# Kernel optimization log

Hardware: AMD Instinct MI355X
Metric: run time of the kernel (lower is better)

The kernel has to match this reference:

```python
import jax, jax.numpy as jnp
import numpy as np

B, T = 2, 1024
V, D, H, L = 32000, 1024, 16, 8
DH = D // H  # 64
ROPE_BASE = 1000.0
EPS = 1e-6


def _rms_norm(x):
    # F.rms_norm(x, (C,), eps=1e-6)
    ms = jnp.mean(jnp.square(x), axis=-1, keepdims=True)
    return x * jax.lax.rsqrt(ms + EPS)


def _rope_tables(t_len):
    quarter = DH // 4
    inv_freq = jnp.concatenate([
        ROPE_BASE ** (-jnp.arange(quarter, dtype=jnp.float32) / quarter),
        jnp.zeros(quarter, dtype=jnp.float32),
    ])  # [DH/2]
    theta = jnp.arange(t_len, dtype=jnp.float32)[:, None] * inv_freq[None, :]  # [T, DH/2]
    return jnp.cos(theta), jnp.sin(theta)


def _apply_rope(x, cos, sin):
    # x: [B, H, T, DH]; cos/sin: [T, DH/2] broadcast to [1,1,T,DH/2]
    half = DH // 2
    x1, x2 = x[..., :half], x[..., half:]
    c = cos[None, None]
    s = sin[None, None]
    return jnp.concatenate([c * x1 - s * x2, s * x1 + c * x2], axis=-1).astype(x.dtype)


def setup_inputs() -> dict:
    key = jax.random.key(0)
    ks = jax.random.split(key, 7)
    s = 0.02
    return {
        "x_indices": jax.random.randint(ks[0], (B, T), 0, V, dtype=jnp.int32),
        "embedding": jax.random.normal(ks[1], (V, D), dtype=jnp.float32) * s,
        "Wqkv": jax.random.normal(ks[2], (L, 3 * D, D), dtype=jnp.float32) * s,
        "Wout": jax.random.normal(ks[3], (L, D, D), dtype=jnp.float32) * s,
        "W1": jax.random.normal(ks[4], (L, 4 * D, D), dtype=jnp.float32) * s,
        "W2": jax.random.normal(ks[5], (L, D, 4 * D), dtype=jnp.float32) * s,
        "lm_head": jax.random.normal(ks[6], (V, D), dtype=jnp.float32) * s,
    }


def reference(x_indices, embedding, Wqkv, Wout, W1, W2, lm_head):
    x = embedding[x_indices]  # [B, T, D]
    cos, sin = _rope_tables(T)
    causal = jnp.tril(jnp.ones((T, T), dtype=bool))  # [T, T]
    neg = jnp.finfo(x.dtype).min
    scale = 1.0 / np.sqrt(DH)

    for l in range(L):
        n = _rms_norm(x)
        qkv = jnp.einsum('btd,ed->bte', n, Wqkv[l])  # [B, T, 3D]
        qkv = qkv.reshape(B, T, 3, H, DH)
        q = jnp.transpose(qkv[:, :, 0], (0, 2, 1, 3))  # [B, H, T, DH]
        k = jnp.transpose(qkv[:, :, 1], (0, 2, 1, 3))
        v = jnp.transpose(qkv[:, :, 2], (0, 2, 1, 3))
        q = _apply_rope(q, cos, sin)
        k = _apply_rope(k, cos, sin)
        scores = jnp.einsum('bhqd,bhkd->bhqk', q, k) * scale
        scores = jnp.where(causal[None, None], scores, neg)
        attn = jax.nn.softmax(scores, axis=-1)
        ctx = jnp.einsum('bhqk,bhkd->bhqd', attn, v)
        ctx = jnp.transpose(ctx, (0, 2, 1, 3)).reshape(B, T, D)
        x = x + jnp.einsum('btd,ed->bte', ctx, Wout[l])
        n = _rms_norm(x)
        h = jnp.square(jax.nn.relu(jnp.einsum('btd,fd->btf', n, W1[l])))  # [B, T, 4D]
        x = x + jnp.einsum('btf,df->btd', h, W2[l])

    logits = jnp.einsum('btd,vd->btv', _rms_norm(x), lm_head)
    return logits.astype(jnp.float32)
```

## Files before the change

### kernel.cpp

```cpp
#include <hip/hip_runtime.h>
#include <hip/hip_bf16.h>
#include <cmath>
#include <cstdint>

#define B_  2
#define T_  1024
#define V_  32000
#define D_  1024
#define H_  16
#define L_  8
#define DH_ 64

typedef __attribute__((ext_vector_type(8))) short bf16x8;
typedef __attribute__((ext_vector_type(4))) float f32x4;

__device__ __forceinline__ ushort f2bf(float f) {
    union { float f; uint32_t u; } v; v.f = f;
    uint32_t r = v.u + 0x7FFFu + ((v.u >> 16) & 1u);
    return (ushort)(r >> 16);
}
__device__ __forceinline__ float bf2f(ushort u) {
    union { uint32_t u; float f; } v; v.u = ((uint32_t)u) << 16;
    return v.f;
}

__device__ __forceinline__ void async_copy16(const void* g, void* l) {
    __builtin_amdgcn_global_load_lds(
        (const __attribute__((address_space(1))) void*)g,
        (__attribute__((address_space(3))) void*)l, 16, 0, 0);
}

__global__ __launch_bounds__(256) void k_cast(const float4* __restrict__ in,
                                              ushort4* __restrict__ out, int n4) {
    for (int i = blockIdx.x * 256 + threadIdx.x; i < n4; i += gridDim.x * 256) {
        float4 v = in[i];
        out[i] = make_ushort4(f2bf(v.x), f2bf(v.y), f2bf(v.z), f2bf(v.w));
    }
}

__global__ void k_rope_tables(float* __restrict__ cosT, float* __restrict__ sinT) {
    int t = blockIdx.x;
    int i = threadIdx.x;
    float invf = (i < 16) ? powf(1000.0f, -(float)i / 16.0f) : 0.0f;
    float th = (float)t * invf;
    cosT[t * 32 + i] = cosf(th);
    sinT[t * 32 + i] = sinf(th);
}

__global__ __launch_bounds__(256) void k_gather(const int* __restrict__ idx,
                                                const float* __restrict__ emb,
                                                float* __restrict__ x) {
    int row = blockIdx.x;
    int id = idx[row];
    const float4* src = (const float4*)(emb + (size_t)id * D_);
    float4* dst = (float4*)(x + (size_t)row * D_);
    dst[threadIdx.x] = src[threadIdx.x];
}

__global__ __launch_bounds__(256) void k_rmsnorm(const float* __restrict__ x,
                                                 ushort* __restrict__ out) {
    int row = blockIdx.x;
    const float4* xr = (const float4*)(x + (size_t)row * D_);
    float4 v = xr[threadIdx.x];
    float ss = v.x * v.x + v.y * v.y + v.z * v.z + v.w * v.w;
    #pragma unroll
    for (int off = 1; off < 64; off <<= 1) ss += __shfl_xor(ss, off);
    __shared__ float wsum[4];
    int lane = threadIdx.x & 63, wv = threadIdx.x >> 6;
    if (lane == 0) wsum[wv] = ss;
    __syncthreads();
    float tot = wsum[0] + wsum[1] + wsum[2] + wsum[3];
    float inv = rsqrtf(tot * (1.0f / D_) + 1e-6f);
    ushort4 r = make_ushort4(f2bf(v.x * inv), f2bf(v.y * inv), f2bf(v.z * inv), f2bf(v.w * inv));
    *(ushort4*)(out + (size_t)row * D_ + threadIdx.x * 4) = r;
}

template<int BN, int EPI, bool OUTBF, bool CONVB>
__global__ __launch_bounds__(256) void k_mfma_gemm(const ushort* __restrict__ A,
                                                   const void* __restrict__ Wp,
                                                   void* __restrict__ Cp,
                                                   const float* __restrict__ Res,
                                                   const float* __restrict__ cosT,
                                                   const float* __restrict__ sinT,
                                                   int M, int N, int K) {
    constexpr int BM = 128;
    constexpr int MI = 4;
    constexpr int NI = BN / 32;
    __shared__ ushort As[BM][64];
    __shared__ ushort Bs[BN][64];
    const int tid = threadIdx.x;
    const int wid = tid >> 6, lane = tid & 63;
    const int wr = wid >> 1, wc = wid & 1;
    const int r16 = lane & 15, kc = lane >> 4;
    const int rx = (r16 & 7) << 4;
    const size_t bm = (size_t)blockIdx.x * BM;
    const size_t bn = (size_t)blockIdx.y * BN;
    const int srow = tid >> 3;
    const int sdcp = tid & 7;

    f32x4 acc[MI][NI];
    #pragma unroll
    for (int mi = 0; mi < MI; mi++)
        #pragma unroll
        for (int ni = 0; ni < NI; ni++) {
            f32x4 z = {0.f, 0.f, 0.f, 0.f};
            acc[mi][ni] = z;
        }

    for (int k0 = 0; k0 < K; k0 += 64) {
        #pragma unroll
        for (int i = 0; i < 4; i++) {
            const int row = i * 32 + srow;
            const ushort* g = A + (bm + row) * (size_t)K + k0 + ((sdcp ^ (row & 7)) * 8);
            async_copy16(g, (char*)As + (i * 256 + tid) * 16);
        }
        if constexpr (!CONVB) {
            const ushort* Wb = (const ushort*)Wp;
            #pragma unroll
            for (int i = 0; i < BN / 32; i++) {
                const int row = i * 32 + srow;
                const ushort* g = Wb + (bn + row) * (size_t)K + k0 + ((sdcp ^ (row & 7)) * 8);
                async_copy16(g, (char*)Bs + (i * 256 + tid) * 16);
            }
        } else {
            const float* Wf = (const float*)Wp;
            #pragma unroll
            for (int i = 0; i < BN / 32; i++) {
                const int row = i * 32 + srow;
                const float* src = Wf + (bn + row) * (size_t)K + k0 + sdcp * 8;
                float4 v0 = *(const float4*)(src);
                float4 v1 = *(const float4*)(src + 4);
                union { ushort u[8]; bf16x8 v; } tmp;
                tmp.u[0] = f2bf(v0.x); tmp.u[1] = f2bf(v0.y);
                tmp.u[2] = f2bf(v0.z); tmp.u[3] = f2bf(v0.w);
                tmp.u[4] = f2bf(v1.x); tmp.u[5] = f2bf(v1.y);
                tmp.u[6] = f2bf(v1.z); tmp.u[7] = f2bf(v1.w);
                *(bf16x8*)((char*)Bs + row * 128 + ((sdcp ^ (row & 7)) << 4)) = tmp.v;
            }
        }
        __syncthreads();

        #pragma unroll
        for (int kk = 0; kk < 2; kk++) {
            bf16x8 af[MI], bfr[NI];
            #pragma unroll
            for (int mi = 0; mi < MI; mi++)
                af[mi] = *(const bf16x8*)((const char*)As + (wr * 64 + mi * 16 + r16) * 128 +
                                          ((kk * 64 + kc * 16) ^ rx));
            #pragma unroll
            for (int ni = 0; ni < NI; ni++)
                bfr[ni] = *(const bf16x8*)((const char*)Bs + (wc * (BN / 2) + ni * 16 + r16) * 128 +
                                           ((kk * 64 + kc * 16) ^ rx));
            #pragma unroll
            for (int mi = 0; mi < MI; mi++)
                #pragma unroll
                for (int ni = 0; ni < NI; ni++)
                    acc[mi][ni] = __builtin_amdgcn_mfma_f32_16x16x32_bf16(af[mi], bfr[ni],
                                                                          acc[mi][ni], 0, 0, 0);
        }
        __syncthreads();
    }

    #pragma unroll
    for (int mi = 0; mi < MI; mi++) {
        #pragma unroll
        for (int j = 0; j < 4; j++) {
            const size_t row = bm + wr * 64 + mi * 16 + (lane >> 4) * 4 + j;
            if constexpr (EPI == 3) {
                static_assert(BN == 128, "rope epilogue assumes BN=128");
                const int sec = (int)((bn + wc * 64) >> 10);
                if (sec < 2) {
                    const int t = (int)(row & (T_ - 1));
                    #pragma unroll
                    for (int np = 0; np < 2; np++) {
                        const int i1 = np * 16 + r16;
                        float c = cosT[t * 32 + i1], s = sinT[t * 32 + i1];
                        float x1 = acc[mi][np][j], x2 = acc[mi][np + 2][j];
                        acc[mi][np][j]     = c * x1 - s * x2;
                        acc[mi][np + 2][j] = s * x1 + c * x2;
                    }
                }
            }
            #pragma unroll
            for (int ni = 0; ni < NI; ni++) {
                const size_t col = bn + wc * (BN / 2) + ni * 16 + r16;
                float v = acc[mi][ni][j];
                if constexpr (EPI == 1) v += Res[row * N + col];
                if constexpr (EPI == 2) { v = fmaxf(v, 0.f); v *= v; }
                if constexpr (OUTBF) ((ushort*)Cp)[row * N + col] = f2bf(v);
                else                 ((float*)Cp)[row * N + col] = v;
            }
        }
    }
}

__global__ __launch_bounds__(256) void k_attn_mfma(const ushort* __restrict__ qkv,
                                                   ushort* __restrict__ ctx) {
    __shared__ __align__(16) char lds[24576];
    const int tid = threadIdx.x;
    const int w = tid >> 6, lane = tid & 63;
    const int r16 = lane & 15, kc = lane >> 4;
    const int qb = blockIdx.x * 64;
    const int bh = blockIdx.y, b = bh >> 4, h = bh & 15;
    const size_t tok0 = (size_t)b * T_;
    const ushort* qg = qkv + (tok0 + qb) * (3 * D_) + h * DH_;
    const ushort* kg = qkv + tok0 * (3 * D_) + D_ + h * DH_;
    const ushort* vg = qkv + tok0 * (3 * D_) + 2 * D_ + h * DH_;
    const float SCALE_LOG2E = 0.125f * 1.44269504089f;

    #pragma unroll
    for (int i = 0; i < 2; i++) {
        int slot = i * 256 + tid;
        int row = slot >> 3, dcp = slot & 7;
        int d0 = (dcp ^ (row & 7)) * 8;
        async_copy16(qg + (size_t)row * (3 * D_) + d0, lds + 16384 + slot * 16);
    }
    __syncthreads();
    bf16x8 aq[2];
    #pragma unroll
    for (int ks = 0; ks < 2; ks++) {
        int row = w * 16 + r16;
        aq[ks] = *(const bf16x8*)(lds + 16384 + row * 128 + ((ks * 64 + kc * 16) ^ ((row & 7) << 4)));
    }

    f32x4 o[4];
    float m[4], l[4], corr[4];
    #pragma unroll
    for (int nd = 0; nd < 4; nd++) { f32x4 z = {0.f, 0.f, 0.f, 0.f}; o[nd] = z; }
    #pragma unroll
    for (int j = 0; j < 4; j++) { m[j] = -1e30f; l[j] = 0.f; }

    const int nch = (qb >> 6) + 1;
    for (int ch = 0; ch < nch; ch++) {
        const int kb = ch << 6;
        __syncthreads();
        #pragma unroll
        for (int i = 0; i < 2; i++) {
            int slot = i * 256 + tid;
            int row = slot >> 3, dcp = slot & 7;
            int d0 = (dcp ^ (row & 7)) * 8;
            async_copy16(kg + (size_t)(kb + row) * (3 * D_) + d0, lds + slot * 16);
        }
        {
            int key = tid >> 2, dbase = (tid & 3) * 16;
            const ushort* src = vg + (size_t)(kb + key) * (3 * D_) + dbase;
            bf16x8 v0 = *(const bf16x8*)(src);
            bf16x8 v1 = *(const bf16x8*)(src + 8);
            #pragma unroll
            for (int e = 0; e < 8; e++) {
                int d = dbase + e;
                *(ushort*)(lds + 8192 + d * 128 + ((key * 2) ^ ((d & 7) << 4))) = (ushort)v0[e];
                d = dbase + 8 + e;
                *(ushort*)(lds + 8192 + d * 128 + ((key * 2) ^ ((d & 7) << 4))) = (ushort)v1[e];
            }
        }
        __syncthreads();

        f32x4 s[4];
        #pragma unroll
        for (int ni = 0; ni < 4; ni++) { f32x4 z = {0.f, 0.f, 0.f, 0.f}; s[ni] = z; }
        __builtin_amdgcn_s_setprio(1);
        #pragma unroll
        for (int ks = 0; ks < 2; ks++)
            #pragma unroll
            for (int ni = 0; ni < 4; ni++) {
                int row = ni * 16 + r16;
                bf16x8 kf = *(const bf16x8*)(lds + row * 128 + ((ks * 64 + kc * 16) ^ ((row & 7) << 4)));
                s[ni] = __builtin_amdgcn_mfma_f32_16x16x32_bf16(aq[ks], kf, s[ni], 0, 0, 0);
            }
        __builtin_amdgcn_s_setprio(0);

        const bool diag = (kb == qb);
        #pragma unroll
        for (int j = 0; j < 4; j++) {
            const int qrow = qb + w * 16 + kc * 4 + j;
            #pragma unroll
            for (int ni = 0; ni < 4; ni++) {
                float v = s[ni][j] * SCALE_LOG2E;
                if (diag) { int key = kb + ni * 16 + r16; if (key > qrow) v = -1e30f; }
                s[ni][j] = v;
            }
            float t = fmaxf(fmaxf(s[0][j], s[1][j]), fmaxf(s[2][j], s[3][j]));
            #pragma unroll
            for (int off = 1; off < 16; off <<= 1) t = fmaxf(t, __shfl_xor(t, off));
            float mn = fmaxf(m[j], t);
            corr[j] = exp2f(m[j] - mn);
            m[j] = mn;
            float ps = 0.f;
            #pragma unroll
            for (int ni = 0; ni < 4; ni++) {
                float p = exp2f(s[ni][j] - mn);
                s[ni][j] = p;
                ps += p;
            }
            #pragma unroll
            for (int off = 1; off < 16; off <<= 1) ps += __shfl_xor(ps, off);
            l[j] = l[j] * corr[j] + ps;
        }
        #pragma unroll
        for (int ni = 0; ni < 4; ni++)
            #pragma unroll
            for (int j = 0; j < 4; j++) {
                int row = w * 16 + kc * 4 + j;
                *(ushort*)(lds + 16384 + row * 128 + ((ni * 32 + r16 * 2) ^ ((row & 7) << 4))) = f2bf(s[ni][j]);
            }
        #pragma unroll
        for (int nd = 0; nd < 4; nd++)
            #pragma unroll
            for (int j = 0; j < 4; j++) o[nd][j] *= corr[j];
        __builtin_amdgcn_s_setprio(1);
        #pragma unroll
        for (int ks = 0; ks < 2; ks++) {
            int prow = w * 16 + r16;
            bf16x8 pf = *(const bf16x8*)(lds + 16384 + prow * 128 + ((ks * 64 + kc * 16) ^ ((prow & 7) << 4)));
            #pragma unroll
            for (int nd = 0; nd < 4; nd++) {
                int drow = nd * 16 + r16;
                bf16x8 vf = *(const bf16x8*)(lds + 8192 + drow * 128 + ((ks * 64 + kc * 16) ^ ((drow & 7) << 4)));
                o[nd] = __builtin_amdgcn_mfma_f32_16x16x32_bf16(pf, vf, o[nd], 0, 0, 0);
            }
        }
        __builtin_amdgcn_s_setprio(0);
    }

    #pragma unroll
    for (int j = 0; j < 4; j++) {
        float inv = 1.0f / l[j];
        int row = qb + w * 16 + kc * 4 + j;
        ushort* dst = ctx + (tok0 + row) * D_ + h * DH_;
        #pragma unroll
        for (int nd = 0; nd < 4; nd++)
            dst[nd * 16 + r16] = f2bf(o[nd][j] * inv);
    }
}

extern "C" void kernel_launch(void* const* d_in, const int* in_sizes, int n_in,
                              void* d_out, int out_size, void* d_ws, size_t ws_size,
                              hipStream_t stream) {
    const int*   xi   = (const int*)d_in[0];
    const float* emb  = (const float*)d_in[1];
    const float* Wqkv = (const float*)d_in[2];
    const float* Wout = (const float*)d_in[3];
    const float* W1   = (const float*)d_in[4];
    const float* W2   = (const float*)d_in[5];
    const float* lmh  = (const float*)d_in[6];
    float* out = (float*)d_out;

    const size_t NT = (size_t)B_ * T_;
    size_t off = 0;
    auto carve = [&](size_t bytes) -> char* {
        char* r = (char*)d_ws + off;
        off += (bytes + 255) & ~(size_t)255;
        return r;
    };
    float*  xbuf = (float*)carve(NT * D_ * 4);
    ushort* qkv  = (ushort*)carve(NT * 3 * D_ * 2);
    ushort* nb   = (ushort*)carve(NT * D_ * 2);
    ushort* ctxb = (ushort*)carve(NT * D_ * 2);
    ushort* hb   = (ushort*)carve(NT * 4 * D_ * 2);
    float*  cosT = (float*)carve(T_ * 32 * 4);
    float*  sinT = (float*)carve(T_ * 32 * 4);

    const size_t nWqkv = (size_t)L_ * 3 * D_ * D_;
    const size_t nWout = (size_t)L_ * D_ * D_;
    const size_t nW1   = (size_t)L_ * 4 * D_ * D_;
    const size_t nW2   = (size_t)L_ * 4 * D_ * D_;
    const size_t nLmh  = (size_t)V_ * D_;
    ushort* WqkvB = (ushort*)carve(nWqkv * 2);
    ushort* WoutB = (ushort*)carve(nWout * 2);
    ushort* W1B   = (ushort*)carve(nW1 * 2);
    ushort* W2B   = (ushort*)carve(nW2 * 2);
    ushort* lmhB  = (ushort*)carve(nLmh * 2);
    const bool preconv = (off <= ws_size);

    if (preconv) {
        k_cast<<<dim3(2048), dim3(256), 0, stream>>>((const float4*)Wqkv, (ushort4*)WqkvB, (int)(nWqkv / 4));
        k_cast<<<dim3(2048), dim3(256), 0, stream>>>((const float4*)Wout, (ushort4*)WoutB, (int)(nWout / 4));
        k_cast<<<dim3(2048), dim3(256), 0, stream>>>((const float4*)W1,   (ushort4*)W1B,   (int)(nW1 / 4));
        k_cast<<<dim3(2048), dim3(256), 0, stream>>>((const float4*)W2,   (ushort4*)W2B,   (int)(nW2 / 4));
        k_cast<<<dim3(2048), dim3(256), 0, stream>>>((const float4*)lmh,  (ushort4*)lmhB,  (int)(nLmh / 4));
    }

#define LAUNCH_GEMM(BN, EPI, OUTBF, GX, GY, Aq, Wb16, Wf32, Cq, Rq, Mv, Nv, Kv)              \
    do {                                                                                     \
        if (preconv)                                                                         \
            k_mfma_gemm<BN, EPI, OUTBF, false><<<dim3(GX, GY), dim3(256), 0, stream>>>(      \
                (const ushort*)(Aq), (const void*)(Wb16), (void*)(Cq), (Rq), cosT, sinT,     \
                Mv, Nv, Kv);                                                                 \
        else                                                                                 \
            k_mfma_gemm<BN, EPI, OUTBF, true><<<dim3(GX, GY), dim3(256), 0, stream>>>(       \
                (const ushort*)(Aq), (const void*)(Wf32), (void*)(Cq), (Rq), cosT, sinT,     \
                Mv, Nv, Kv);                                                                 \
    } while (0)

    k_rope_tables<<<dim3(T_), dim3(32), 0, stream>>>(cosT, sinT);
    k_gather<<<dim3(NT), dim3(256), 0, stream>>>(xi, emb, xbuf);

    for (int l = 0; l < L_; l++) {
        k_rmsnorm<<<dim3(NT), dim3(256), 0, stream>>>(xbuf, nb);
        LAUNCH_GEMM(128, 3, true, 16, 24, nb,
                    WqkvB + (size_t)l * 3 * D_ * D_, Wqkv + (size_t)l * 3 * D_ * D_,
                    qkv, nullptr, (int)NT, 3 * D_, D_);
        k_attn_mfma<<<dim3(T_ / 64, B_ * H_), dim3(256), 0, stream>>>(qkv, ctxb);
        LAUNCH_GEMM(64, 1, false, 16, 16, ctxb,
                    WoutB + (size_t)l * D_ * D_, Wout + (size_t)l * D_ * D_,
                    xbuf, xbuf, (int)NT, D_, D_);
        k_rmsnorm<<<dim3(NT), dim3(256), 0, stream>>>(xbuf, nb);
        LAUNCH_GEMM(128, 2, true, 16, 32, nb,
                    W1B + (size_t)l * 4 * D_ * D_, W1 + (size_t)l * 4 * D_ * D_,
                    hb, nullptr, (int)NT, 4 * D_, D_);
        LAUNCH_GEMM(64, 1, false, 16, 16, hb,
                    W2B + (size_t)l * 4 * D_ * D_, W2 + (size_t)l * 4 * D_ * D_,
                    xbuf, xbuf, (int)NT, D_, 4 * D_);
    }
    k_rmsnorm<<<dim3(NT), dim3(256), 0, stream>>>(xbuf, nb);
    LAUNCH_GEMM(128, 0, false, 16, 250, nb, lmhB, lmh, out, nullptr, (int)NT, V_, D_);
#undef LAUNCH_GEMM
}
```

Measured before the change: 1.995 ms.

## Double-buffer GEMM LDS tiles, swizzle workgroup order, nontemporal fp32 output stores

The MFMA GEMM now uses two LDS buffers per operand and issues the next K-tile's loads before computing on the current one, so global-to-LDS traffic can overlap with MFMA work. Workgroup IDs are remapped in groups of eight to change which tiles run at the same time, aiming for better L2 reuse. Plain fp32 outputs (EPI 0, such as the logits) are written with nontemporal stores to avoid polluting the cache. The cost is double the LDS use, which can lower occupancy.

```diff
diff --git a/kernel.cpp b/kernel.cpp
--- a/kernel.cpp
+++ b/kernel.cpp
@@ -86,47 +86,42 @@
     constexpr int BM = 128;
     constexpr int MI = 4;
     constexpr int NI = BN / 32;
-    __shared__ ushort As[BM][64];
-    __shared__ ushort Bs[BN][64];
+    __shared__ ushort As[2][BM][64];
+    __shared__ ushort Bs[2][BN][64];
     const int tid = threadIdx.x;
     const int wid = tid >> 6, lane = tid & 63;
     const int wr = wid >> 1, wc = wid & 1;
     const int r16 = lane & 15, kc = lane >> 4;
     const int rx = (r16 & 7) << 4;
-    const size_t bm = (size_t)blockIdx.x * BM;
-    const size_t bn = (size_t)blockIdx.y * BN;
-    const int srow = tid >> 3;
+    const int srow8 = tid >> 3;
     const int sdcp = tid & 7;
 
-    f32x4 acc[MI][NI];
-    #pragma unroll
-    for (int mi = 0; mi < MI; mi++)
-        #pragma unroll
-        for (int ni = 0; ni < NI; ni++) {
-            f32x4 z = {0.f, 0.f, 0.f, 0.f};
-            acc[mi][ni] = z;
-        }
-
-    for (int k0 = 0; k0 < K; k0 += 64) {
+    const int nwg = gridDim.x * gridDim.y;
+    int orig = blockIdx.y * gridDim.x + blockIdx.x;
+    int swz = (nwg & 7) ? orig : ((orig & 7) * (nwg >> 3) + (orig >> 3));
+    const size_t bm = (size_t)(swz % gridDim.x) * BM;
+    const size_t bn = (size_t)(swz / gridDim.x) * BN;
+
+    auto stage = [&](int buf, int k0) {
         #pragma unroll
         for (int i = 0; i < 4; i++) {
-            const int row = i * 32 + srow;
+            const int row = i * 32 + srow8;
             const ushort* g = A + (bm + row) * (size_t)K + k0 + ((sdcp ^ (row & 7)) * 8);
-            async_copy16(g, (char*)As + (i * 256 + tid) * 16);
+            async_copy16(g, (char*)As + buf * (BM * 128) + (i * 256 + tid) * 16);
         }
         if constexpr (!CONVB) {
             const ushort* Wb = (const ushort*)Wp;
             #pragma unroll
             for (int i = 0; i < BN / 32; i++) {
-                const int row = i * 32 + srow;
+                const int row = i * 32 + srow8;
                 const ushort* g = Wb + (bn + row) * (size_t)K + k0 + ((sdcp ^ (row & 7)) * 8);
-                async_copy16(g, (char*)Bs + (i * 256 + tid) * 16);
+                async_copy16(g, (char*)Bs + buf * (BN * 128) + (i * 256 + tid) * 16);
             }
         } else {
             const float* Wf = (const float*)Wp;
             #pragma unroll
             for (int i = 0; i < BN / 32; i++) {
-                const int row = i * 32 + srow;
+                const int row = i * 32 + srow8;
                 const float* src = Wf + (bn + row) * (size_t)K + k0 + sdcp * 8;
                 float4 v0 = *(const float4*)(src);
                 float4 v1 = *(const float4*)(src + 4);
@@ -135,21 +130,38 @@
                 tmp.u[2] = f2bf(v0.z); tmp.u[3] = f2bf(v0.w);
                 tmp.u[4] = f2bf(v1.x); tmp.u[5] = f2bf(v1.y);
                 tmp.u[6] = f2bf(v1.z); tmp.u[7] = f2bf(v1.w);
-                *(bf16x8*)((char*)Bs + row * 128 + ((sdcp ^ (row & 7)) << 4)) = tmp.v;
-            }
-        }
-        __syncthreads();
-
+                *(bf16x8*)((char*)Bs + buf * (BN * 128) + row * 128 + ((sdcp ^ (row & 7)) << 4)) = tmp.v;
+            }
+        }
+    };
+
+    f32x4 acc[MI][NI];
+    #pragma unroll
+    for (int mi = 0; mi < MI; mi++)
+        #pragma unroll
+        for (int ni = 0; ni < NI; ni++) {
+            f32x4 z = {0.f, 0.f, 0.f, 0.f};
+            acc[mi][ni] = z;
+        }
+
+    const int KSTEPS = K >> 6;
+    stage(0, 0);
+    __syncthreads();
+    for (int step = 0; step < KSTEPS; ++step) {
+        const int cur = step & 1;
+        if (step + 1 < KSTEPS) stage(cur ^ 1, (step + 1) << 6);
         #pragma unroll
         for (int kk = 0; kk < 2; kk++) {
             bf16x8 af[MI], bfr[NI];
             #pragma unroll
             for (int mi = 0; mi < MI; mi++)
-                af[mi] = *(const bf16x8*)((const char*)As + (wr * 64 + mi * 16 + r16) * 128 +
+                af[mi] = *(const bf16x8*)((const char*)As + cur * (BM * 128) +
+                                          (wr * 64 + mi * 16 + r16) * 128 +
                                           ((kk * 64 + kc * 16) ^ rx));
             #pragma unroll
             for (int ni = 0; ni < NI; ni++)
-                bfr[ni] = *(const bf16x8*)((const char*)Bs + (wc * (BN / 2) + ni * 16 + r16) * 128 +
+                bfr[ni] = *(const bf16x8*)((const char*)Bs + cur * (BN * 128) +
+                                           (wc * (BN / 2) + ni * 16 + r16) * 128 +
                                            ((kk * 64 + kc * 16) ^ rx));
             #pragma unroll
             for (int mi = 0; mi < MI; mi++)
@@ -187,8 +199,13 @@
                 float v = acc[mi][ni][j];
                 if constexpr (EPI == 1) v += Res[row * N + col];
                 if constexpr (EPI == 2) { v = fmaxf(v, 0.f); v *= v; }
-                if constexpr (OUTBF) ((ushort*)Cp)[row * N + col] = f2bf(v);
-                else                 ((float*)Cp)[row * N + col] = v;
+                if constexpr (OUTBF) {
+                    ((ushort*)Cp)[row * N + col] = f2bf(v);
+                } else if constexpr (EPI == 0) {
+                    __builtin_nontemporal_store(v, (float*)Cp + row * N + col);
+                } else {
+                    ((float*)Cp)[row * N + col] = v;
+                }
             }
         }
     }
```

New measurement: 1.986 ms. About the same (-0.5%).
